# Optimization experiments

Hardware: AMD Instinct MI355X
Metric: run time of the kernel (lower is better)

Reference implementation:

```python
import jax, jax.numpy as jnp
import numpy as np

B, S, D, H = 4, 2048, 1024, 16
HD = D // H


def setup_inputs() -> dict:
    key = jax.random.key(0)
    k1, k2, k3 = jax.random.split(key, 3)
    x = jax.random.normal(k1, (B, S, D), dtype=jnp.float32)
    # xavier-ish scaling for stable softmax
    W_attn = jax.random.normal(k2, (3 * D, D), dtype=jnp.float32) * (1.0 / np.sqrt(2 * D))
    b_attn = jnp.zeros((3 * D,), dtype=jnp.float32)
    W_out = jax.random.normal(k3, (D, D), dtype=jnp.float32) * (1.0 / np.sqrt(D))
    b_out = jnp.zeros((D,), dtype=jnp.float32)
    return {"x": x, "W_attn": W_attn, "b_attn": b_attn, "W_out": W_out, "b_out": b_out}


def reference(x, W_attn, b_attn, W_out, b_out):
    bs, seq, d = x.shape
    # fused QKV projection (torch Linear: y = x @ W.T + b)
    kqv = jnp.einsum("bsd,ed->bse", x, W_attn) + b_attn
    # NOTE: source splits as k, q, v (k first)
    k, q, v = jnp.split(kqv, 3, axis=2)
    # [b, s, h, hd] -> [b, h, s, hd]
    k = k.reshape(bs, seq, H, HD).transpose(0, 2, 1, 3)
    q = q.reshape(bs, seq, H, HD).transpose(0, 2, 1, 3)
    v = v.reshape(bs, seq, H, HD).transpose(0, 2, 1, 3)
    scale = 1.0 / np.sqrt(HD)
    scores = jnp.einsum("bhqd,bhkd->bhqk", q, k) * scale
    attn = jax.nn.softmax(scores, axis=-1)
    y = jnp.einsum("bhqk,bhkd->bhqd", attn, v)
    y = y.transpose(0, 2, 1, 3).reshape(bs, seq, d)
    out = jnp.einsum("bsd,ed->bse", y, W_out) + b_out
    return out
```

## Files before the change

### kernel.cpp

```cpp
#include <hip/hip_runtime.h>

typedef unsigned short u16;
typedef unsigned int u32;
typedef __attribute__((ext_vector_type(2))) u32 u32x2;
typedef __attribute__((ext_vector_type(4))) u32 u32x4;
typedef __attribute__((ext_vector_type(8))) short bf16x8;
typedef __attribute__((ext_vector_type(4))) short bf16x4;
typedef __attribute__((ext_vector_type(4))) float f32x4;

__device__ __forceinline__ u16 f2bf(float f) {
  u32 b = __float_as_uint(f);
  b += 0x7fffu + ((b >> 16) & 1u);
  return (u16)(b >> 16);
}

__device__ __forceinline__ u32 pk2bf(float a, float b) {
#if __has_builtin(__builtin_amdgcn_cvt_pk_bf16_f32)
  return __builtin_bit_cast(u32, __builtin_amdgcn_cvt_pk_bf16_f32(a, b));
#else
  return (u32)f2bf(a) | ((u32)f2bf(b) << 16);
#endif
}

__device__ __forceinline__ bf16x4 mk_bf16x4(u32 lo, u32 hi) {
  u32x2 t;
  t[0] = lo;
  t[1] = hi;
  return __builtin_bit_cast(bf16x4, t);
}

__device__ __forceinline__ float fexp2(float x) {
#if __has_builtin(__builtin_amdgcn_exp2f)
  return __builtin_amdgcn_exp2f(x);
#else
  return exp2f(x);
#endif
}

__device__ __forceinline__ f32x4 mfma16x16x16(bf16x4 a, bf16x4 b, f32x4 c) {
#if __has_builtin(__builtin_amdgcn_mfma_f32_16x16x16bf16_1k)
  return __builtin_amdgcn_mfma_f32_16x16x16bf16_1k(a, b, c, 0, 0, 0);
#elif __has_builtin(__builtin_amdgcn_mfma_f32_16x16x16_bf16)
  return __builtin_amdgcn_mfma_f32_16x16x16_bf16(a, b, c, 0, 0, 0);
#else
  asm volatile("v_mfma_f32_16x16x16_bf16 %0, %1, %2, %0\n\ts_nop 7\n\ts_nop 7"
               : "+v"(c)
               : "v"(a), "v"(b));
  return c;
#endif
}

__device__ __forceinline__ void gload_lds16(const u16* g, u16* l) {
  __builtin_amdgcn_global_load_lds((const __attribute__((address_space(1))) void*)g,
                                   (__attribute__((address_space(3))) void*)l, 16, 0, 0);
}

__global__ __launch_bounds__(256) void cvt_f32_bf16(const float* __restrict__ in,
                                                    u16* __restrict__ out) {
  long i = ((long)blockIdx.x * 256 + threadIdx.x) * 8;
  u32 u[8];
#pragma unroll
  for (int j = 0; j < 8; j++) {
    u32 b = __float_as_uint(in[i + j]);
    u[j] = (b + 0x7fffu + ((b >> 16) & 1u)) >> 16;
  }
  u32x4 o;
  o[0] = u[0] | (u[1] << 16);
  o[1] = u[2] | (u[3] << 16);
  o[2] = u[4] | (u[5] << 16);
  o[3] = u[6] | (u[7] << 16);
  *(u32x4*)(out + i) = o;
}

__device__ __forceinline__ void gemm_core_128(const u16* __restrict__ A,
                                              const u16* __restrict__ B, int K,
                                              int m0, int n0, u16* As, u16* Bs,
                                              f32x4 acc[4][4]) {
  int t = threadIdx.x;
  int lane = t & 63, w = t >> 6;
  int quad = lane >> 4, l16 = lane & 15;
  int wm = (w >> 1) * 64, wn = (w & 1) * 64;
  int lr = lane >> 3, lc = lane & 7;
  int cg = lc ^ lr;
  int swz = l16 & 7;
  for (int k0 = 0; k0 < K; k0 += 64) {
#pragma unroll
    for (int i = 0; i < 4; i++) {
      int r0 = i * 32 + w * 8;
      gload_lds16(&A[(long)(m0 + r0 + lr) * K + k0 + cg * 8], &As[r0 * 64]);
      gload_lds16(&B[(long)(n0 + r0 + lr) * K + k0 + cg * 8], &Bs[r0 * 64]);
    }
    __syncthreads();
#pragma unroll
    for (int ks = 0; ks < 2; ks++) {
      bf16x8 a[4], b[4];
#pragma unroll
      for (int tm = 0; tm < 4; tm++)
        a[tm] = *(const bf16x8*)&As[(wm + tm * 16 + l16) * 64 + ((ks * 4 + quad) ^ swz) * 8];
#pragma unroll
      for (int tn = 0; tn < 4; tn++)
        b[tn] = *(const bf16x8*)&Bs[(wn + tn * 16 + l16) * 64 + ((ks * 4 + quad) ^ swz) * 8];
#pragma unroll
      for (int tm = 0; tm < 4; tm++)
#pragma unroll
        for (int tn = 0; tn < 4; tn++)
          acc[tm][tn] = __builtin_amdgcn_mfma_f32_16x16x32_bf16(a[tm], b[tn],
                                                                acc[tm][tn], 0, 0, 0);
    }
    __syncthreads();
  }
}

#define QSCALE 0.1803368801f
__global__ __launch_bounds__(256) void gemm_qkv(const u16* __restrict__ A,
                                                const u16* __restrict__ B,
                                                const float* __restrict__ bias,
                                                u16* __restrict__ Kg,
                                                u16* __restrict__ Qg,
                                                u16* __restrict__ Vg) {
  __shared__ __align__(16) u16 As[128 * 64];
  __shared__ __align__(16) u16 Bs[128 * 64];
  const int K = 1024;
  int m0 = blockIdx.y * 128, n0 = blockIdx.x * 128;
  f32x4 acc[4][4];
#pragma unroll
  for (int i = 0; i < 4; i++)
#pragma unroll
    for (int j = 0; j < 4; j++) acc[i][j] = (f32x4)0.0f;
  gemm_core_128(A, B, K, m0, n0, As, Bs, acc);

  int t = threadIdx.x, lane = t & 63, w = t >> 6;
  int quad = lane >> 4, l16 = lane & 15;
  int wm = (w >> 1) * 64, wn = (w & 1) * 64;
#pragma unroll
  for (int tn = 0; tn < 4; tn++) {
    int n = n0 + wn + tn * 16 + l16;
    float bv = bias[n];
    int which = n >> 10;
    int h = (n >> 6) & 15, d = n & 63;
#pragma unroll
    for (int tm = 0; tm < 4; tm++) {
      int m = m0 + wm + tm * 16 + quad * 4;
      int b = m >> 11, s = m & 2047;
      long bh = (long)b * 16 + h;
      if (which == 2) {
        u32x2 pk;
        pk[0] = pk2bf(acc[tm][tn][0] + bv, acc[tm][tn][1] + bv);
        pk[1] = pk2bf(acc[tm][tn][2] + bv, acc[tm][tn][3] + bv);
        *(u32x2*)&Vg[(bh * 64 + d) * 2048 + s] = pk;
      } else {
#pragma unroll
        for (int r = 0; r < 4; r++) {
          float v = acc[tm][tn][r] + bv;
          if (which == 0)
            Kg[(bh * 2048 + s + r) * 64 + d] = f2bf(v);
          else
            Qg[(bh * 2048 + s + r) * 64 + d] = f2bf(v * QSCALE);
        }
      }
    }
  }
}

__global__ __launch_bounds__(256) void gemm_out(const u16* __restrict__ A,
                                                const u16* __restrict__ B,
                                                const float* __restrict__ bias,
                                                float* __restrict__ out) {
  __shared__ __align__(16) u16 As[128 * 64];
  __shared__ __align__(16) u16 Bs[128 * 64];
  const int K = 1024, N = 1024;
  int m0 = blockIdx.y * 128, n0 = blockIdx.x * 128;
  f32x4 acc[4][4];
#pragma unroll
  for (int i = 0; i < 4; i++)
#pragma unroll
    for (int j = 0; j < 4; j++) acc[i][j] = (f32x4)0.0f;
  gemm_core_128(A, B, K, m0, n0, As, Bs, acc);

  int t = threadIdx.x, lane = t & 63, w = t >> 6;
  int quad = lane >> 4, l16 = lane & 15;
  int wm = (w >> 1) * 64, wn = (w & 1) * 64;
#pragma unroll
  for (int tn = 0; tn < 4; tn++) {
    int n = n0 + wn + tn * 16 + l16;
    float bv = bias[n];
#pragma unroll
    for (int tm = 0; tm < 4; tm++) {
#pragma unroll
      for (int r = 0; r < 4; r++) {
        int m = m0 + wm + tm * 16 + quad * 4 + r;
        out[(long)m * N + n] = acc[tm][tn][r] + bv;
      }
    }
  }
}

#define SYNC_V4                                          \
  __builtin_amdgcn_sched_barrier(0);                     \
  asm volatile("s_waitcnt vmcnt(4)" ::: "memory");       \
  __builtin_amdgcn_s_barrier();                          \
  __builtin_amdgcn_sched_barrier(0)

#define SYNC_V0                                          \
  __builtin_amdgcn_sched_barrier(0);                     \
  asm volatile("s_waitcnt vmcnt(0)" ::: "memory");       \
  __builtin_amdgcn_s_barrier();                          \
  __builtin_amdgcn_sched_barrier(0)

#define STAGE_KV(tt, bb)                                                       \
  do {                                                                         \
    const u16* kp_ = Kbase + (long)(tt)*4096;                                  \
    const u16* vp_ = Vbase + (tt)*64;                                          \
    gload_lds16(kp_ + (w * 8) * 64, &Ks3[bb][(w * 8) * 64]);                   \
    gload_lds16(kp_ + (w * 8 + 32) * 64, &Ks3[bb][(w * 8 + 32) * 64]);         \
    gload_lds16(vp_ + (long)(w * 8) * 2048, &Vs3[bb][(w * 8) * 64]);           \
    gload_lds16(vp_ + (long)(w * 8 + 32) * 2048, &Vs3[bb][(w * 8 + 32) * 64]); \
  } while (0)

#define COMPUTE(bb)                                                            \
  do {                                                                         \
    const u16* Kc_ = Ks3[bb];                                                  \
    const u16* Vc_ = Vs3[bb];                                                  \
    bf16x8 kf_[4][2];                                                          \
    _Pragma("unroll") for (int tn = 0; tn < 4; tn++)                           \
        _Pragma("unroll") for (int ks = 0; ks < 2; ks++)                       \
            kf_[tn][ks] = *(const bf16x8*)&Kc_[(tn * 16 + l16) * 64 +          \
                                               ((ks * 4 + quad) ^ swz) * 8];   \
    bf16x4 pf_[2][4];                                                          \
    _Pragma("unroll") for (int tq = 0; tq < 2; tq++) {                         \
      f32x4 s_[4];                                                             \
      __builtin_amdgcn_s_setprio(1);                                           \
      _Pragma("unroll") for (int tn = 0; tn < 4; tn++)                         \
          s_[tn] = __builtin_amdgcn_mfma_f32_16x16x32_bf16(                    \
              kf_[tn][0], qf[tq][0], Z, 0, 0, 0);                              \
      _Pragma("unroll") for (int tn = 0; tn < 4; tn++)                         \
          s_[tn] = __builtin_amdgcn_mfma_f32_16x16x32_bf16(                    \
              kf_[tn][1], qf[tq][1], s_[tn], 0, 0, 0);                         \
      __builtin_amdgcn_s_setprio(0);                                           \
      _Pragma("unroll") for (int tn = 0; tn < 4; tn++) {                       \
        float e0 = fexp2(s_[tn][0]);                                           \
        float e1 = fexp2(s_[tn][1]);                                           \
        float e2 = fexp2(s_[tn][2]);                                           \
        float e3 = fexp2(s_[tn][3]);                                           \
        pf_[tq][tn] = mk_bf16x4(pk2bf(e0, e1), pk2bf(e2, e3));                 \
      }                                                                        \
    }                                                                          \
    __builtin_amdgcn_s_setprio(1);                                             \
    _Pragma("unroll") for (int tn = 0; tn < 4; tn++) {                         \
      bf16x4 vf_[4];                                                           \
      _Pragma("unroll") for (int dt = 0; dt < 4; dt++)                         \
          vf_[dt] = *(const bf16x4*)&Vc_[(dt * 16 + l16) * 64 +                \
                                         ((tn * 2 + (quad >> 1)) ^ swz) * 8 +  \
                                         (quad & 1) * 4];                      \
      acc_sum[0] = mfma16x16x16(ONES, pf_[0][tn], acc_sum[0]);                 \
      acc_sum[1] = mfma16x16x16(ONES, pf_[1][tn], acc_sum[1]);                 \
      _Pragma("unroll") for (int tq = 0; tq < 2; tq++)                         \
          _Pragma("unroll") for (int dt = 0; dt < 4; dt++)                     \
              acc[dt][tq] = mfma16x16x16(vf_[dt], pf_[tq][tn], acc[dt][tq]);   \
    }                                                                          \
    __builtin_amdgcn_s_setprio(0);                                             \
  } while (0)

__global__ __launch_bounds__(256, 3) void attn_kernel(const u16* __restrict__ Qg,
                                                      const u16* __restrict__ Kg,
                                                      const u16* __restrict__ Vg,
                                                      u16* __restrict__ Y) {
  __shared__ __align__(16) u16 Ks3[3][64 * 64];
  __shared__ __align__(16) u16 Vs3[3][64 * 64];
  int t = threadIdx.x, lane = t & 63, w = t >> 6;
  int quad = lane >> 4, l16 = lane & 15;
  int bh = blockIdx.y;
  int q0 = blockIdx.x * 128 + w * 32;
  int lr = lane >> 3, lc = lane & 7, cg = lc ^ lr;
  int swz = l16 & 7;

  bf16x8 qf[2][2];
#pragma unroll
  for (int tq = 0; tq < 2; tq++) {
    const u16* qp = Qg + ((long)bh * 2048 + q0 + tq * 16 + l16) * 64;
    qf[tq][0] = *(const bf16x8*)(qp + quad * 8);
    qf[tq][1] = *(const bf16x8*)(qp + 32 + quad * 8);
  }

  const f32x4 Z = {0.0f, 0.0f, 0.0f, 0.0f};
  const bf16x4 ONES = mk_bf16x4(0x3F803F80u, 0x3F803F80u);

  f32x4 acc[4][2];
  f32x4 acc_sum[2];
#pragma unroll
  for (int dt = 0; dt < 4; dt++)
#pragma unroll
    for (int tq = 0; tq < 2; tq++) acc[dt][tq] = (f32x4)0.0f;
  acc_sum[0] = (f32x4)0.0f;
  acc_sum[1] = (f32x4)0.0f;

  const u16* Kbase = Kg + ((long)bh * 2048 + lr) * 64 + cg * 8;
  const u16* Vbase = Vg + ((long)bh * 64 + lr) * 2048 + cg * 8;

  STAGE_KV(0, 0);
  STAGE_KV(1, 1);

  for (int base = 0; base < 30; base += 3) {
    SYNC_V4;
    STAGE_KV(base + 2, 2);
    COMPUTE(0);
    SYNC_V4;
    STAGE_KV(base + 3, 0);
    COMPUTE(1);
    SYNC_V4;
    STAGE_KV(base + 4, 1);
    COMPUTE(2);
  }
  SYNC_V4;
  COMPUTE(0);
  SYNC_V0;
  COMPUTE(1);

  int b = bh >> 4, h = bh & 15;
#pragma unroll
  for (int tq = 0; tq < 2; tq++) {
    float inv = 1.0f / acc_sum[tq][0];
    long row = (long)b * 2048 + q0 + tq * 16 + l16;
#pragma unroll
    for (int dt = 0; dt < 4; dt++) {
      u32x2 pk;
      pk[0] = pk2bf(acc[dt][tq][0] * inv, acc[dt][tq][1] * inv);
      pk[1] = pk2bf(acc[dt][tq][2] * inv, acc[dt][tq][3] * inv);
      *(u32x2*)&Y[row * 1024 + h * 64 + dt * 16 + quad * 4] = pk;
    }
  }
}

extern "C" void kernel_launch(void* const* d_in, const int* in_sizes, int n_in,
                              void* d_out, int out_size, void* d_ws, size_t ws_size,
                              hipStream_t stream) {
  const float* x = (const float*)d_in[0];
  const float* W_attn = (const float*)d_in[1];
  const float* b_attn = (const float*)d_in[2];
  const float* W_out = (const float*)d_in[3];
  const float* b_out = (const float*)d_in[4];
  float* out = (float*)d_out;

  char* ws = (char*)d_ws;
  u16* xb = (u16*)ws;
  u16* Wab = (u16*)(ws + 16777216);
  u16* Wob = (u16*)(ws + 16777216 + 6291456);
  u16* Kg = (u16*)(ws + 25165824);
  u16* Qg = Kg + 8388608;
  u16* Vg = Qg + 8388608;
  u16* Yb = xb;

  cvt_f32_bf16<<<4096, 256, 0, stream>>>(x, xb);
  cvt_f32_bf16<<<1536, 256, 0, stream>>>(W_attn, Wab);
  cvt_f32_bf16<<<512, 256, 0, stream>>>(W_out, Wob);

  gemm_qkv<<<dim3(24, 64), 256, 0, stream>>>(xb, Wab, b_attn, Kg, Qg, Vg);
  attn_kernel<<<dim3(16, 64), 256, 0, stream>>>(Qg, Kg, Vg, Yb);
  gemm_out<<<dim3(8, 64), 256, 0, stream>>>(Yb, Wob, b_out, out);
}
```

Baseline: 298.1 us.

## Restructure attention: 512-thread blocks, P via LDS, 16x16x32 MFMA for PV

The attention kernel now runs 512-thread blocks of 8 waves covering 256 queries, so each staged K/V tile is shared by twice as many waves. The K/V ring drops from three buffers to two, with a full vmcnt(0) wait at every barrier. The exp'd probabilities are written to a per-wave LDS scratch and read back in the layout the 16x16x32 bf16 MFMA expects, which replaces the 16x16x16 MFMAs for the PV product and the row sums. This halves the PV MFMA count and the per-thread staging loads, at the cost of an extra LDS round-trip for P, shallower prefetch, and more LDS per block.

```diff
diff --git a/kernel.cpp b/kernel.cpp
--- a/kernel.cpp
+++ b/kernel.cpp
@@ -22,11 +22,10 @@
 #endif
 }
 
-__device__ __forceinline__ bf16x4 mk_bf16x4(u32 lo, u32 hi) {
-  u32x2 t;
-  t[0] = lo;
-  t[1] = hi;
-  return __builtin_bit_cast(bf16x4, t);
+__device__ __forceinline__ bf16x8 mk_ones8() {
+  u32x4 t;
+  t[0] = t[1] = t[2] = t[3] = 0x3F803F80u;
+  return __builtin_bit_cast(bf16x8, t);
 }
 
 __device__ __forceinline__ float fexp2(float x) {
@@ -34,19 +33,6 @@
   return __builtin_amdgcn_exp2f(x);
 #else
   return exp2f(x);
-#endif
-}
-
-__device__ __forceinline__ f32x4 mfma16x16x16(bf16x4 a, bf16x4 b, f32x4 c) {
-#if __has_builtin(__builtin_amdgcn_mfma_f32_16x16x16bf16_1k)
-  return __builtin_amdgcn_mfma_f32_16x16x16bf16_1k(a, b, c, 0, 0, 0);
-#elif __has_builtin(__builtin_amdgcn_mfma_f32_16x16x16_bf16)
-  return __builtin_amdgcn_mfma_f32_16x16x16_bf16(a, b, c, 0, 0, 0);
-#else
-  asm volatile("v_mfma_f32_16x16x16_bf16 %0, %1, %2, %0\n\ts_nop 7\n\ts_nop 7"
-               : "+v"(c)
-               : "v"(a), "v"(b));
-  return c;
 #endif
 }
 
@@ -195,84 +181,86 @@
   }
 }
 
-#define SYNC_V4                                          \
-  __builtin_amdgcn_sched_barrier(0);                     \
-  asm volatile("s_waitcnt vmcnt(4)" ::: "memory");       \
-  __builtin_amdgcn_s_barrier();                          \
+#define SYNC                                       \
+  __builtin_amdgcn_sched_barrier(0);               \
+  asm volatile("s_waitcnt vmcnt(0)" ::: "memory"); \
+  __builtin_amdgcn_s_barrier();                    \
   __builtin_amdgcn_sched_barrier(0)
 
-#define SYNC_V0                                          \
-  __builtin_amdgcn_sched_barrier(0);                     \
-  asm volatile("s_waitcnt vmcnt(0)" ::: "memory");       \
-  __builtin_amdgcn_s_barrier();                          \
-  __builtin_amdgcn_sched_barrier(0)
-
-#define STAGE_KV(tt, bb)                                                       \
-  do {                                                                         \
-    const u16* kp_ = Kbase + (long)(tt)*4096;                                  \
-    const u16* vp_ = Vbase + (tt)*64;                                          \
-    gload_lds16(kp_ + (w * 8) * 64, &Ks3[bb][(w * 8) * 64]);                   \
-    gload_lds16(kp_ + (w * 8 + 32) * 64, &Ks3[bb][(w * 8 + 32) * 64]);         \
-    gload_lds16(vp_ + (long)(w * 8) * 2048, &Vs3[bb][(w * 8) * 64]);           \
-    gload_lds16(vp_ + (long)(w * 8 + 32) * 2048, &Vs3[bb][(w * 8 + 32) * 64]); \
+#define STAGE_KV(tt, bb)                                      \
+  do {                                                        \
+    gload_lds16(Kst + (long)(tt)*4096, &Ks[bb][w * 8 * 64]);  \
+    gload_lds16(Vst + (tt)*64, &Vs[bb][w * 8 * 64]);          \
   } while (0)
 
 #define COMPUTE(bb)                                                            \
   do {                                                                         \
-    const u16* Kc_ = Ks3[bb];                                                  \
-    const u16* Vc_ = Vs3[bb];                                                  \
-    bf16x8 kf_[4][2];                                                          \
-    _Pragma("unroll") for (int tn = 0; tn < 4; tn++)                           \
-        _Pragma("unroll") for (int ks = 0; ks < 2; ks++)                       \
-            kf_[tn][ks] = *(const bf16x8*)&Kc_[(tn * 16 + l16) * 64 +          \
-                                               ((ks * 4 + quad) ^ swz) * 8];   \
-    bf16x4 pf_[2][4];                                                          \
+    bf16x8 pf_[2][2];                                                          \
     _Pragma("unroll") for (int tq = 0; tq < 2; tq++) {                         \
       f32x4 s_[4];                                                             \
       __builtin_amdgcn_s_setprio(1);                                           \
-      _Pragma("unroll") for (int tn = 0; tn < 4; tn++)                         \
-          s_[tn] = __builtin_amdgcn_mfma_f32_16x16x32_bf16(                    \
-              kf_[tn][0], qf[tq][0], Z, 0, 0, 0);                              \
-      _Pragma("unroll") for (int tn = 0; tn < 4; tn++)                         \
-          s_[tn] = __builtin_amdgcn_mfma_f32_16x16x32_bf16(                    \
-              kf_[tn][1], qf[tq][1], s_[tn], 0, 0, 0);                         \
+      _Pragma("unroll") for (int tn = 0; tn < 4; tn++) {                       \
+        bf16x8 kf0 = *(const bf16x8*)(kL0 + (bb)*4096 + tn * 1024);            \
+        bf16x8 kf1 = *(const bf16x8*)(kL1 + (bb)*4096 + tn * 1024);            \
+        s_[tn] = __builtin_amdgcn_mfma_f32_16x16x32_bf16(kf0, qf[tq][0], Z,    \
+                                                         0, 0, 0);             \
+        s_[tn] = __builtin_amdgcn_mfma_f32_16x16x32_bf16(kf1, qf[tq][1],       \
+                                                         s_[tn], 0, 0, 0);     \
+      }                                                                        \
       __builtin_amdgcn_s_setprio(0);                                           \
       _Pragma("unroll") for (int tn = 0; tn < 4; tn++) {                       \
         float e0 = fexp2(s_[tn][0]);                                           \
         float e1 = fexp2(s_[tn][1]);                                           \
         float e2 = fexp2(s_[tn][2]);                                           \
         float e3 = fexp2(s_[tn][3]);                                           \
-        pf_[tq][tn] = mk_bf16x4(pk2bf(e0, e1), pk2bf(e2, e3));                 \
+        u32x2 pk;                                                              \
+        pk[0] = pk2bf(e0, e1);                                                 \
+        pk[1] = pk2bf(e2, e3);                                                 \
+        *(u32x2*)(pW + tq * 1024 + woff[tn]) = pk;                             \
       }                                                                        \
     }                                                                          \
+    _Pragma("unroll") for (int ks = 0; ks < 2; ks++)                           \
+        _Pragma("unroll") for (int tq = 0; tq < 2; tq++) {                     \
+      u32x2 lo = *(const u32x2*)(pR + tq * 1024 + prlo[ks]);                   \
+      u32x2 hi = *(const u32x2*)(pR + tq * 1024 + prhi[ks]);                   \
+      u32x4 cc;                                                                \
+      cc[0] = lo[0];                                                           \
+      cc[1] = lo[1];                                                           \
+      cc[2] = hi[0];                                                           \
+      cc[3] = hi[1];                                                           \
+      pf_[tq][ks] = __builtin_bit_cast(bf16x8, cc);                            \
+    }                                                                          \
     __builtin_amdgcn_s_setprio(1);                                             \
-    _Pragma("unroll") for (int tn = 0; tn < 4; tn++) {                         \
-      bf16x4 vf_[4];                                                           \
-      _Pragma("unroll") for (int dt = 0; dt < 4; dt++)                         \
-          vf_[dt] = *(const bf16x4*)&Vc_[(dt * 16 + l16) * 64 +                \
-                                         ((tn * 2 + (quad >> 1)) ^ swz) * 8 +  \
-                                         (quad & 1) * 4];                      \
-      acc_sum[0] = mfma16x16x16(ONES, pf_[0][tn], acc_sum[0]);                 \
-      acc_sum[1] = mfma16x16x16(ONES, pf_[1][tn], acc_sum[1]);                 \
-      _Pragma("unroll") for (int tq = 0; tq < 2; tq++)                         \
-          _Pragma("unroll") for (int dt = 0; dt < 4; dt++)                     \
-              acc[dt][tq] = mfma16x16x16(vf_[dt], pf_[tq][tn], acc[dt][tq]);   \
+    _Pragma("unroll") for (int ks = 0; ks < 2; ks++) {                         \
+      acc_sum[0] = __builtin_amdgcn_mfma_f32_16x16x32_bf16(ONES, pf_[0][ks],   \
+                                                           acc_sum[0], 0, 0, 0); \
+      acc_sum[1] = __builtin_amdgcn_mfma_f32_16x16x32_bf16(ONES, pf_[1][ks],   \
+                                                           acc_sum[1], 0, 0, 0); \
+      _Pragma("unroll") for (int dt = 0; dt < 4; dt++) {                       \
+        bf16x8 vf = *(const bf16x8*)(vL[ks] + (bb)*4096 + dt * 1024);          \
+        acc[dt][0] = __builtin_amdgcn_mfma_f32_16x16x32_bf16(vf, pf_[0][ks],   \
+                                                             acc[dt][0], 0, 0, 0); \
+        acc[dt][1] = __builtin_amdgcn_mfma_f32_16x16x32_bf16(vf, pf_[1][ks],   \
+                                                             acc[dt][1], 0, 0, 0); \
+      }                                                                        \
     }                                                                          \
     __builtin_amdgcn_s_setprio(0);                                             \
   } while (0)
 
-__global__ __launch_bounds__(256, 3) void attn_kernel(const u16* __restrict__ Qg,
+__global__ __launch_bounds__(512, 4) void attn_kernel(const u16* __restrict__ Qg,
                                                       const u16* __restrict__ Kg,
                                                       const u16* __restrict__ Vg,
                                                       u16* __restrict__ Y) {
-  __shared__ __align__(16) u16 Ks3[3][64 * 64];
-  __shared__ __align__(16) u16 Vs3[3][64 * 64];
+  __shared__ __align__(16) u16 Ks[2][64 * 64];
+  __shared__ __align__(16) u16 Vs[2][64 * 64];
+  __shared__ __align__(16) u16 Ps[8 * 32 * 64];
   int t = threadIdx.x, lane = t & 63, w = t >> 6;
   int quad = lane >> 4, l16 = lane & 15;
   int bh = blockIdx.y;
-  int q0 = blockIdx.x * 128 + w * 32;
+  int q0 = blockIdx.x * 256 + w * 32;
   int lr = lane >> 3, lc = lane & 7, cg = lc ^ lr;
   int swz = l16 & 7;
+  u16* Pw = Ps + w * 2048;
 
   bf16x8 qf[2][2];
 #pragma unroll
@@ -283,7 +271,7 @@
   }
 
   const f32x4 Z = {0.0f, 0.0f, 0.0f, 0.0f};
-  const bf16x4 ONES = mk_bf16x4(0x3F803F80u, 0x3F803F80u);
+  const bf16x8 ONES = mk_ones8();
 
   f32x4 acc[4][2];
   f32x4 acc_sum[2];
@@ -294,26 +282,37 @@
   acc_sum[0] = (f32x4)0.0f;
   acc_sum[1] = (f32x4)0.0f;
 
-  const u16* Kbase = Kg + ((long)bh * 2048 + lr) * 64 + cg * 8;
-  const u16* Vbase = Vg + ((long)bh * 64 + lr) * 2048 + cg * 8;
+  const u16* kL0 = &Ks[0][l16 * 64 + (quad ^ swz) * 8];
+  const u16* kL1 = &Ks[0][l16 * 64 + ((4 + quad) ^ swz) * 8];
+  const u16* vL[2] = {&Vs[0][l16 * 64 + (quad ^ swz) * 8],
+                      &Vs[0][l16 * 64 + ((4 + quad) ^ swz) * 8]};
+  u16* pW = Pw + l16 * 64;
+  const u16* pR = Pw + l16 * 64;
+  int woff[4], prlo[2], prhi[2];
+#pragma unroll
+  for (int tn = 0; tn < 4; tn++) woff[tn] = ((tn * 4 + quad) ^ l16) * 4;
+#pragma unroll
+  for (int ks = 0; ks < 2; ks++) {
+    prlo[ks] = ((ks * 8 + quad * 2) ^ l16) * 4;
+    prhi[ks] = ((ks * 8 + quad * 2 + 1) ^ l16) * 4;
+  }
+
+  const u16* Kst = Kg + ((long)bh * 2048 + w * 8 + lr) * 64 + cg * 8;
+  const u16* Vst = Vg + ((long)(bh * 64 + w * 8 + lr)) * 2048 + cg * 8;
 
   STAGE_KV(0, 0);
-  STAGE_KV(1, 1);
-
-  for (int base = 0; base < 30; base += 3) {
-    SYNC_V4;
-    STAGE_KV(base + 2, 2);
+  for (int tt = 0; tt < 30; tt += 2) {
+    SYNC;
+    STAGE_KV(tt + 1, 1);
     COMPUTE(0);
-    SYNC_V4;
-    STAGE_KV(base + 3, 0);
+    SYNC;
+    STAGE_KV(tt + 2, 0);
     COMPUTE(1);
-    SYNC_V4;
-    STAGE_KV(base + 4, 1);
-    COMPUTE(2);
-  }
-  SYNC_V4;
+  }
+  SYNC;
+  STAGE_KV(31, 1);
   COMPUTE(0);
-  SYNC_V0;
+  SYNC;
   COMPUTE(1);
 
   int b = bh >> 4, h = bh & 15;
@@ -355,6 +354,6 @@
   cvt_f32_bf16<<<512, 256, 0, stream>>>(W_out, Wob);
 
   gemm_qkv<<<dim3(24, 64), 256, 0, stream>>>(xb, Wab, b_attn, Kg, Qg, Vg);
-  attn_kernel<<<dim3(16, 64), 256, 0, stream>>>(Qg, Kg, Vg, Yb);
+  attn_kernel<<<dim3(8, 64), 512, 0, stream>>>(Qg, Kg, Vg, Yb);
   gemm_out<<<dim3(8, 64), 256, 0, stream>>>(Yb, Wob, b_out, out);
 }
```

New measurement: 292.7 us. No clear change (-1.8%).
